# Performance work log

Hardware: AMD Instinct MI355X
Metric: run time of the kernel (lower is better)

The kernel has to match this reference:

```python
import jax, jax.numpy as jnp
import numpy as np

N = 100000
E = 1600000
IN_C = 128
HID = 32
HEADS = 4
NUM_CLASSES = 16
NEG_SLOPE = 0.2


def setup_inputs() -> dict:
    key = jax.random.key(0)
    ks = jax.random.split(key, 10)
    x = jax.random.normal(ks[0], (N, IN_C), dtype=jnp.float32)
    edge_index = jax.random.randint(ks[1], (2, E), 0, N, dtype=jnp.int32)
    s1 = 1.0 / np.sqrt(IN_C)
    s2 = 1.0 / np.sqrt(HID * HEADS)
    W1 = jax.random.normal(ks[2], (IN_C, HEADS * HID), dtype=jnp.float32) * s1
    att_src1 = jax.random.normal(ks[3], (HEADS, HID), dtype=jnp.float32) * s1
    att_dst1 = jax.random.normal(ks[4], (HEADS, HID), dtype=jnp.float32) * s1
    b1 = jnp.zeros((HEADS * HID,), dtype=jnp.float32)
    W2 = jax.random.normal(ks[5], (HEADS * HID, NUM_CLASSES), dtype=jnp.float32) * s2
    att_src2 = jax.random.normal(ks[6], (1, NUM_CLASSES), dtype=jnp.float32) * s2
    att_dst2 = jax.random.normal(ks[7], (1, NUM_CLASSES), dtype=jnp.float32) * s2
    b2 = jnp.zeros((NUM_CLASSES,), dtype=jnp.float32)
    return {"x": x, "edge_index": edge_index,
            "W1": W1, "att_src1": att_src1, "att_dst1": att_dst1, "b1": b1,
            "W2": W2, "att_src2": att_src2, "att_dst2": att_dst2, "b2": b2}


def _gat_conv(x, src, dst, W, att_src, att_dst, b):
    # PyG GATConv: shared linear for src/dst, additive attention, segment softmax over dst.
    n = x.shape[0]
    H, C = att_src.shape
    h = (x @ W).reshape(n, H, C)                       # [N, H, C]
    a_s = jnp.einsum('nhc,hc->nh', h, att_src)          # [N, H]
    a_d = jnp.einsum('nhc,hc->nh', h, att_dst)          # [N, H]
    e = a_s[src] + a_d[dst]                             # [E, H]
    e = jnp.where(e >= 0, e, NEG_SLOPE * e)             # leaky_relu(0.2)
    # numerically stable segment softmax over destination node groups
    e_max = jax.ops.segment_max(e, dst, num_segments=n)
    e_exp = jnp.exp(e - e_max[dst])
    denom = jax.ops.segment_sum(e_exp, dst, num_segments=n)
    alpha = e_exp / denom[dst]                          # [E, H]
    msg = h[src] * alpha[:, :, None]                    # [E, H, C]
    out = jax.ops.segment_sum(msg, dst, num_segments=n) # [N, H, C]
    return out.reshape(n, H * C) + b


def reference(x, edge_index, W1, att_src1, att_dst1, b1, W2, att_src2, att_dst2, b2):
    n = x.shape[0]
    # add_self_loops=True (PyG default), same augmented edge set for both layers
    loop = jnp.arange(n, dtype=edge_index.dtype)
    src = jnp.concatenate([edge_index[0], loop])
    dst = jnp.concatenate([edge_index[1], loop])
    h = _gat_conv(x, src, dst, W1, att_src1, att_dst1, b1)
    h = jax.nn.elu(h)
    out = _gat_conv(h, src, dst, W2, att_src2, att_dst2, b2)
    return out
```

## Files before the change

kernel.cpp:

```cpp
#include <hip/hip_runtime.h>
#include <hip/hip_bf16.h>
#include <math.h>


typedef unsigned short u16;
typedef unsigned int u32;
typedef __attribute__((ext_vector_type(8))) short bf16x8;
typedef __attribute__((ext_vector_type(4))) float f32x4;

__device__ __forceinline__ float eluf(float v) { return v > 0.f ? v : expm1f(v); }
__device__ __forceinline__ u16 f2bf(float f) {
    u32 u = __float_as_uint(f);
    u += 0x7fff + ((u >> 16) & 1);
    return (u16)(u >> 16);
}
__device__ __forceinline__ float bf2f(u16 u) {
    return __uint_as_float(((u32)u) << 16);
}
__device__ __forceinline__ float expleaky(float e) {
    float m = e >= 0.f ? 1.44269504f : 0.28853901f;
    return exp2f(e * m);
}

__global__ __launch_bounds__(256) void ksetup(
    const float* __restrict__ W1, const float* __restrict__ W2,
    const float* __restrict__ ats2, const float* __restrict__ atd2,
    u16* __restrict__ w1fh, u16* __restrict__ w1fl,
    float* __restrict__ u, float* __restrict__ v, u16* __restrict__ w2tb,
    int* __restrict__ deg, int N)
{
    const int b = blockIdx.x, tid = threadIdx.x;
    if (b < 64) {
        int idx = b * 256 + tid;
        int j = idx & 7, l = (idx >> 3) & 63, q = (idx >> 9) & 3, ct = idx >> 11;
        int k = q * 32 + (l >> 4) * 8 + j;
        int n = ct * 16 + (l & 15);
        float w = W1[k * 128 + n];
        u16 hv = f2bf(w);
        w1fh[idx] = hv;
        w1fl[idx] = f2bf(w - bf2f(hv));
    } else if (b == 64) {
        if (tid < 128) {
            float su = 0.f, sv = 0.f;
            #pragma unroll
            for (int j = 0; j < 16; ++j) {
                float w = W2[tid * 16 + j];
                su = fmaf(w, ats2[j], su);
                sv = fmaf(w, atd2[j], sv);
                w2tb[j * 128 + tid] = f2bf(w);
            }
            u[tid] = su; v[tid] = sv;
        }
    } else {
        int z = (b - 65) * 1024 + tid * 4;
        if (z < N) *(int4*)&deg[z] = make_int4(0, 0, 0, 0);
    }
}

#define REPSTRIDE 136
__global__ __launch_bounds__(256) void mega1(
    const float* __restrict__ x, const u16* __restrict__ w1fh,
    const u16* __restrict__ w1fl,
    const float* __restrict__ att_s, const float* __restrict__ att_d,
    u16* __restrict__ h1b, float* __restrict__ as1, float* __restrict__ ad1,
    int N,
    const int* __restrict__ ei, int* __restrict__ deg, int* __restrict__ rank,
    int E, int grid)
{
    __shared__ union {
        struct { u16 lh[8192]; u16 ll[8192]; } w;
        u16 rep[16384];
    } sm;
    const int tid = threadIdx.x;

    for (int e = blockIdx.x * 256 + tid; e < E; e += grid * 256) {
        int dd = ei[E + e];
        rank[e] = atomicAdd(&deg[dd], 1);
    }

    const int wv = tid >> 6, lane = tid & 63;
    const int base = blockIdx.x * 64 + wv * 16;
    const int m = lane & 15, quad = lane >> 4;

    int arow = base + m;
    if (arow >= N) arow = 0;
    const float* xr = &x[(size_t)arow * 128 + quad * 8];
    bf16x8 ah[4], al[4];
    #pragma unroll
    for (int q = 0; q < 4; ++q) {
        float4 f0 = *(const float4*)&xr[q * 32];
        float4 f1 = *(const float4*)&xr[q * 32 + 4];
        float fv[8] = {f0.x, f0.y, f0.z, f0.w, f1.x, f1.y, f1.z, f1.w};
        union { u16 us[8]; bf16x8 v; } hh, lu;
        #pragma unroll
        for (int j = 0; j < 8; ++j) {
            u16 h = f2bf(fv[j]);
            hh.us[j] = h;
            lu.us[j] = f2bf(fv[j] - bf2f(h));
        }
        ah[q] = hh.v; al[q] = lu.v;
    }

    f32x4 accs[8];
    for (int p = 0; p < 2; ++p) {
        __syncthreads();
        #pragma unroll
        for (int i = 0; i < 4; ++i) {
            int fi = (tid + i * 256) * 8;
            *(uint4*)&sm.w.lh[fi] = *(const uint4*)&w1fh[p * 8192 + fi];
            *(uint4*)&sm.w.ll[fi] = *(const uint4*)&w1fl[p * 8192 + fi];
        }
        __syncthreads();
        #pragma unroll
        for (int ctl = 0; ctl < 4; ++ctl) {
            f32x4 acc = {0.f, 0.f, 0.f, 0.f};
            #pragma unroll
            for (int q = 0; q < 4; ++q) {
                const int off = ((ctl * 4 + q) * 64 + lane) * 8;
                bf16x8 bh = *(const bf16x8*)&sm.w.lh[off];
                bf16x8 bl = *(const bf16x8*)&sm.w.ll[off];
                acc = __builtin_amdgcn_mfma_f32_16x16x32_bf16(ah[q], bh, acc, 0, 0, 0);
                acc = __builtin_amdgcn_mfma_f32_16x16x32_bf16(al[q], bh, acc, 0, 0, 0);
                acc = __builtin_amdgcn_mfma_f32_16x16x32_bf16(ah[q], bl, acc, 0, 0, 0);
            }
            accs[p * 4 + ctl] = acc;
        }
    }

    #pragma unroll
    for (int h = 0; h < 4; ++h) {
        const float cs0 = att_s[h * 32 + m];
        const float cs1 = att_s[h * 32 + 16 + m];
        const float cd0 = att_d[h * 32 + m];
        const float cd1 = att_d[h * 32 + 16 + m];
        float sp[4], dp[4];
        #pragma unroll
        for (int r = 0; r < 4; ++r) {
            sp[r] = fmaf(accs[2 * h][r], cs0, accs[2 * h + 1][r] * cs1);
            dp[r] = fmaf(accs[2 * h][r], cd0, accs[2 * h + 1][r] * cd1);
        }
        #pragma unroll
        for (int r = 0; r < 4; ++r) {
            sp[r] += __shfl_xor(sp[r], 1); sp[r] += __shfl_xor(sp[r], 2);
            sp[r] += __shfl_xor(sp[r], 4); sp[r] += __shfl_xor(sp[r], 8);
            dp[r] += __shfl_xor(dp[r], 1); dp[r] += __shfl_xor(dp[r], 2);
            dp[r] += __shfl_xor(dp[r], 4); dp[r] += __shfl_xor(dp[r], 8);
        }
        if (m == 0) {
            #pragma unroll
            for (int r = 0; r < 4; ++r) {
                int rr = base + quad * 4 + r;
                if (rr < N) {
                    as1[rr * 4 + h] = sp[r];
                    ad1[rr * 4 + h] = dp[r];
                }
            }
        }
    }

    __syncthreads();
    u16* rep = sm.rep + wv * (16 * REPSTRIDE);
    #pragma unroll
    for (int ct = 0; ct < 8; ++ct) {
        #pragma unroll
        for (int r = 0; r < 4; ++r)
            rep[(quad * 4 + r) * REPSTRIDE + ct * 16 + m] = f2bf(accs[ct][r]);
    }
    const int rr0 = lane >> 2, cc = lane & 3;
    #pragma unroll
    for (int round = 0; round < 4; ++round) {
        int chunk = cc + 4 * round;
        uint4 vv = *(const uint4*)&rep[rr0 * REPSTRIDE + chunk * 8];
        int grow = base + rr0;
        if (grow < N)
            *(uint4*)&h1b[(size_t)grow * 128 + chunk * 8] = vv;
    }
}

__global__ __launch_bounds__(256) void kscan1(
    const int* __restrict__ deg, int* __restrict__ rowptr,
    int* __restrict__ bsum, int N)
{
    __shared__ int lds[256];
    const int t = threadIdx.x;
    const int base = blockIdx.x * 1024 + t * 4;
    int v[4];
    int s = 0;
    #pragma unroll
    for (int j = 0; j < 4; ++j) {
        v[j] = (base + j < N) ? deg[base + j] : 0;
        s += v[j];
    }
    lds[t] = s;
    __syncthreads();
    for (int off = 1; off < 256; off <<= 1) {
        int y = (t >= off) ? lds[t - off] : 0;
        __syncthreads();
        lds[t] += y;
        __syncthreads();
    }
    int run = lds[t] - s;
    #pragma unroll
    for (int j = 0; j < 4; ++j) {
        if (base + j < N) rowptr[base + j] = run;
        run += v[j];
    }
    if (t == 255) bsum[blockIdx.x] = lds[255];
}

__global__ __launch_bounds__(128) void kscan2(int* __restrict__ bsum, int NB)
{
    __shared__ int lds[128];
    const int t = threadIdx.x;
    int v = (t < NB) ? bsum[t] : 0;
    lds[t] = v;
    __syncthreads();
    for (int off = 1; off < 128; off <<= 1) {
        int y = (t >= off) ? lds[t - off] : 0;
        __syncthreads();
        lds[t] += y;
        __syncthreads();
    }
    if (t < NB) bsum[t] = lds[t] - v;
}

__global__ __launch_bounds__(256) void kscat(
    const int* __restrict__ ei, const int* __restrict__ rowptr,
    const int* __restrict__ bsum, const int* __restrict__ rank,
    int* __restrict__ colidx, int E)
{
    int e = blockIdx.x * 256 + threadIdx.x;
    if (e >= E) return;
    int s = ei[e], d = ei[E + e];
    colidx[rowptr[d] + bsum[d >> 10] + rank[e]] = s;
}

__global__ __launch_bounds__(256) void kg1(
    const int* __restrict__ rowptr, const int* __restrict__ bsum,
    const int* __restrict__ colidx,
    const u16* __restrict__ h1b, const float* __restrict__ as1,
    const float* __restrict__ ad1, const float* __restrict__ b1,
    const float* __restrict__ u, const float* __restrict__ v,
    u16* __restrict__ x2b, float* __restrict__ as2, float* __restrict__ ad2,
    int N, int E)
{
    const int d = blockIdx.x * 4 + (threadIdx.x >> 6);
    if (d >= N) return;
    const int lane = threadIdx.x & 63;
    const int c = lane * 2;
    const int headB = lane >> 4;
    const int headA = lane & 3;
    const int eA = lane >> 2;

    const float adA = ad1[d * 4 + headA];
    const float wself = expleaky(as1[d * 4 + headB] + ad1[d * 4 + headB]);
    u32 hd = *(const u32*)&h1b[(d << 7) + c];
    float accx = wself * bf2f((u16)hd);
    float accy = wself * bf2f((u16)(hd >> 16));
    float den = wself;

    int i0r = rowptr[d] + bsum[d >> 10];
    int i1r = (d + 1 == N) ? E : rowptr[d + 1] + bsum[(d + 1) >> 10];
    const int i0 = __builtin_amdgcn_readfirstlane(i0r);
    const int i1 = __builtin_amdgcn_readfirstlane(i1r);

    for (int i = i0; i < i1; i += 16) {
        const int nb = min(16, i1 - i);
        const int ii = i + eA;
        const int iic = ii < i1 ? ii : i0;
        int sAv = colidx[iic];
        float wA = expleaky(as1[(sAv << 2) + headA] + adA);
        wA = (ii < i1) ? wA : 0.f;
        int e = 0;
        for (; e + 8 <= nb; e += 8) {
            int s0 = colidx[i + e + 0];
            int s1 = colidx[i + e + 1];
            int s2 = colidx[i + e + 2];
            int s3 = colidx[i + e + 3];
            int s4 = colidx[i + e + 4];
            int s5 = colidx[i + e + 5];
            int s6 = colidx[i + e + 6];
            int s7 = colidx[i + e + 7];
            float w0 = __shfl(wA, ((e + 0) << 2) + headB);
            float w1 = __shfl(wA, ((e + 1) << 2) + headB);
            float w2 = __shfl(wA, ((e + 2) << 2) + headB);
            float w3 = __shfl(wA, ((e + 3) << 2) + headB);
            float w4 = __shfl(wA, ((e + 4) << 2) + headB);
            float w5 = __shfl(wA, ((e + 5) << 2) + headB);
            float w6 = __shfl(wA, ((e + 6) << 2) + headB);
            float w7 = __shfl(wA, ((e + 7) << 2) + headB);
            u32 v0 = *(const u32*)&h1b[(s0 << 7) + c];
            u32 v1 = *(const u32*)&h1b[(s1 << 7) + c];
            u32 v2 = *(const u32*)&h1b[(s2 << 7) + c];
            u32 v3 = *(const u32*)&h1b[(s3 << 7) + c];
            u32 v4 = *(const u32*)&h1b[(s4 << 7) + c];
            u32 v5 = *(const u32*)&h1b[(s5 << 7) + c];
            u32 v6 = *(const u32*)&h1b[(s6 << 7) + c];
            u32 v7 = *(const u32*)&h1b[(s7 << 7) + c];
            accx = fmaf(w0, bf2f((u16)v0), accx); accy = fmaf(w0, bf2f((u16)(v0 >> 16)), accy);
            accx = fmaf(w1, bf2f((u16)v1), accx); accy = fmaf(w1, bf2f((u16)(v1 >> 16)), accy);
            accx = fmaf(w2, bf2f((u16)v2), accx); accy = fmaf(w2, bf2f((u16)(v2 >> 16)), accy);
            accx = fmaf(w3, bf2f((u16)v3), accx); accy = fmaf(w3, bf2f((u16)(v3 >> 16)), accy);
            accx = fmaf(w4, bf2f((u16)v4), accx); accy = fmaf(w4, bf2f((u16)(v4 >> 16)), accy);
            accx = fmaf(w5, bf2f((u16)v5), accx); accy = fmaf(w5, bf2f((u16)(v5 >> 16)), accy);
            accx = fmaf(w6, bf2f((u16)v6), accx); accy = fmaf(w6, bf2f((u16)(v6 >> 16)), accy);
            accx = fmaf(w7, bf2f((u16)v7), accx); accy = fmaf(w7, bf2f((u16)(v7 >> 16)), accy);
            den += ((w0 + w1) + (w2 + w3)) + ((w4 + w5) + (w6 + w7));
        }
        for (; e < nb; ++e) {
            int s = colidx[i + e];
            float w = __shfl(wA, (e << 2) + headB);
            u32 hv = *(const u32*)&h1b[(s << 7) + c];
            accx = fmaf(w, bf2f((u16)hv), accx);
            accy = fmaf(w, bf2f((u16)(hv >> 16)), accy);
            den += w;
        }
    }

    const float inv = 1.f / den;
    const float2 bv = *(const float2*)&b1[c];
    const float x2a = eluf(fmaf(accx, inv, bv.x));
    const float x2c = eluf(fmaf(accy, inv, bv.y));

    u32 pk = ((u32)f2bf(x2c) << 16) | (u32)f2bf(x2a);
    *(u32*)&x2b[(d << 7) + c] = pk;

    const float2 uv = *(const float2*)&u[c];
    const float2 vv = *(const float2*)&v[c];
    float sA = fmaf(x2a, uv.x, x2c * uv.y);
    float sB = fmaf(x2a, vv.x, x2c * vv.y);
    #pragma unroll
    for (int m = 1; m < 64; m <<= 1) {
        sA += __shfl_xor(sA, m);
        sB += __shfl_xor(sB, m);
    }
    if (lane == 0) { as2[d] = sA; ad2[d] = sB; }
}

__global__ __launch_bounds__(256) void kh2(
    const u16* __restrict__ x2b, const u16* __restrict__ w2tb,
    u16* __restrict__ h2b, int N)
{
    const int wv = threadIdx.x >> 6, lane = threadIdx.x & 63;
    const int n0 = blockIdx.x * 64 + wv * 16;
    if (n0 >= N) return;
    const int m = lane & 15;
    const int kq = lane >> 4;
    bf16x8 bfr[4];
    #pragma unroll
    for (int q = 0; q < 4; ++q)
        bfr[q] = *(const bf16x8*)&w2tb[m * 128 + q * 32 + kq * 8];

    int ar = n0 + m;
    if (ar >= N) ar = N - 1;
    const u16* arow = &x2b[((size_t)ar << 7) + kq * 8];
    f32x4 acc = {0.f, 0.f, 0.f, 0.f};
    #pragma unroll
    for (int q = 0; q < 4; ++q) {
        bf16x8 af = *(const bf16x8*)&arow[q * 32];
        acc = __builtin_amdgcn_mfma_f32_16x16x32_bf16(af, bfr[q], acc, 0, 0, 0);
    }
    #pragma unroll
    for (int r = 0; r < 4; ++r) {
        int rr = n0 + kq * 4 + r;
        if (rr < N) h2b[((size_t)rr << 4) + m] = f2bf(acc[r]);
    }
}

__global__ __launch_bounds__(256) void kg2(
    const int* __restrict__ rowptr, const int* __restrict__ bsum,
    const int* __restrict__ colidx,
    const u16* __restrict__ h2b, const float* __restrict__ as2,
    const float* __restrict__ ad2, const float* __restrict__ b2,
    float* __restrict__ out, int N, int E)
{
    const int d = blockIdx.x * 4 + (threadIdx.x >> 6);
    if (d >= N) return;
    const int lane = threadIdx.x & 63;
    const int ch = lane & 7, g = lane >> 3;

    const float ad_d = ad2[d];
    float acc0 = 0.f, acc1 = 0.f, den = 0.f;
    int i0r = rowptr[d] + bsum[d >> 10];
    int i1r = (d + 1 == N) ? E : rowptr[d + 1] + bsum[(d + 1) >> 10];
    const int i0 = __builtin_amdgcn_readfirstlane(i0r);
    const int i1 = __builtin_amdgcn_readfirstlane(i1r);

    for (int i = i0; i < i1; i += 64) {
        const int nb = min(64, i1 - i);
        const int idx = i + lane;
        const int idxc = idx < i1 ? idx : i0;
        int sA = colidx[idxc];
        float wA = expleaky(as2[sA] + ad_d);
        wA = (idx < i1) ? wA : 0.f;
        const int kU = (nb + 7) >> 3;
        for (int k = 0; k < kU; ++k) {
            int e = g + 8 * k;
            int ec = e < nb ? e : 0;
            float w = __shfl(wA, ec);
            int s = __shfl(sA, ec);
            if (e >= nb) w = 0.f;
            u32 hv = *(const u32*)&h2b[(s << 4) + ch * 2];
            acc0 = fmaf(w, bf2f((u16)hv), acc0);
            acc1 = fmaf(w, bf2f((u16)(hv >> 16)), acc1);
            den += w;
        }
    }
    acc0 += __shfl_xor(acc0, 8); acc0 += __shfl_xor(acc0, 16); acc0 += __shfl_xor(acc0, 32);
    acc1 += __shfl_xor(acc1, 8); acc1 += __shfl_xor(acc1, 16); acc1 += __shfl_xor(acc1, 32);
    den  += __shfl_xor(den, 8);  den  += __shfl_xor(den, 16);  den  += __shfl_xor(den, 32);

    const float wself = expleaky(as2[d] + ad_d);
    u32 hd = *(const u32*)&h2b[(d << 4) + ch * 2];
    acc0 = fmaf(wself, bf2f((u16)hd), acc0);
    acc1 = fmaf(wself, bf2f((u16)(hd >> 16)), acc1);
    den += wself;
    if (g == 0) {
        float2 ov = {acc0 / den + b2[ch * 2], acc1 / den + b2[ch * 2 + 1]};
        *(float2*)&out[(d << 4) + ch * 2] = ov;
    }
}

extern "C" void kernel_launch(void* const* d_in, const int* in_sizes, int n_in,
                              void* d_out, int out_size, void* d_ws, size_t ws_size,
                              hipStream_t stream) {
    const float* x    = (const float*)d_in[0];
    const int*   ei   = (const int*)d_in[1];
    const float* W1   = (const float*)d_in[2];
    const float* ats1 = (const float*)d_in[3];
    const float* atd1 = (const float*)d_in[4];
    const float* b1   = (const float*)d_in[5];
    const float* W2   = (const float*)d_in[6];
    const float* ats2 = (const float*)d_in[7];
    const float* atd2 = (const float*)d_in[8];
    const float* b2   = (const float*)d_in[9];
    float* out = (float*)d_out;
    const int N = in_sizes[0] / 128;
    const int E = in_sizes[1] / 2;

    u16* h1b   = (u16*)d_ws;
    u16* x2b   = h1b + (size_t)N * 128;
    u16* h2b   = x2b + (size_t)N * 128;
    u16* w2tb  = h2b + (size_t)N * 16;
    u16* w1fh  = w2tb + 2048;
    u16* w1fl  = w1fh + 16384;
    float* as1 = (float*)(w1fl + 16384);
    float* ad1 = as1 + (size_t)N * 4;
    float* as2 = ad1 + (size_t)N * 4;
    float* ad2 = as2 + N;
    float* u   = ad2 + N;
    float* v   = u + 128;
    int* deg    = (int*)(v + 128);
    int* rowptr = deg + ((N + 7) & ~3);
    int* bsum   = rowptr + ((N + 7) & ~3);
    int* colidx = bsum + 128;
    int* rank   = colidx + E;

    const int NB  = (N + 1023) / 1024;
    const int Bh1 = (N + 63) / 64;

    hipLaunchKernelGGL(ksetup, dim3(65 + NB), dim3(256), 0, stream,
                       W1, W2, ats2, atd2, w1fh, w1fl, u, v, w2tb, deg, N);
    hipLaunchKernelGGL(mega1, dim3(Bh1), dim3(256), 0, stream,
                       x, w1fh, w1fl, ats1, atd1, h1b, as1, ad1, N,
                       ei, deg, rank, E, Bh1);
    hipLaunchKernelGGL(kscan1, dim3(NB), dim3(256), 0, stream,
                       deg, rowptr, bsum, N);
    hipLaunchKernelGGL(kscan2, dim3(1), dim3(128), 0, stream, bsum, NB);
    hipLaunchKernelGGL(kscat, dim3((E + 255) / 256), dim3(256), 0, stream,
                       ei, rowptr, bsum, rank, colidx, E);
    hipLaunchKernelGGL(kg1, dim3((N + 3) / 4), dim3(256), 0, stream,
                       rowptr, bsum, colidx, h1b, as1, ad1, b1, u, v,
                       x2b, as2, ad2, N, E);
    hipLaunchKernelGGL(kh2, dim3((N + 63) / 64), dim3(256), 0, stream,
                       x2b, w2tb, h2b, N);
    hipLaunchKernelGGL(kg2, dim3((N + 3) / 4), dim3(256), 0, stream,
                       rowptr, bsum, colidx, h2b, as2, ad2, b2, out, N, E);
}
```

Before: 340.5 us.

## Split per-node degree counters into 16 sub-counters to cut atomic contention

Replaces the single per-destination degree counter with 16 sub-counters per node, chosen by edge block, so atomics on the same node are spread out. The scan kernel now prefix-sums the 16 sub-counters per node in place, and the scatter adds the sub-counter offset when it places each edge. The degree-counting loop is also unrolled four ways so loads and atomics are batched, and the h1b store is remapped so each row's chunks are written contiguously. In exchange the counter array grows 16x, which means more zeroing and scan traffic.

```diff
diff --git a/kernel.cpp b/kernel.cpp
--- a/kernel.cpp
+++ b/kernel.cpp
@@ -27,7 +27,7 @@
     const float* __restrict__ ats2, const float* __restrict__ atd2,
     u16* __restrict__ w1fh, u16* __restrict__ w1fl,
     float* __restrict__ u, float* __restrict__ v, u16* __restrict__ w2tb,
-    int* __restrict__ deg, int N)
+    int* __restrict__ degR, int N)
 {
     const int b = blockIdx.x, tid = threadIdx.x;
     if (b < 64) {
@@ -53,7 +53,7 @@
         }
     } else {
         int z = (b - 65) * 1024 + tid * 4;
-        if (z < N) *(int4*)&deg[z] = make_int4(0, 0, 0, 0);
+        if (z < N * 16) *(int4*)&degR[z] = make_int4(0, 0, 0, 0);
     }
 }
 
@@ -64,7 +64,7 @@
     const float* __restrict__ att_s, const float* __restrict__ att_d,
     u16* __restrict__ h1b, float* __restrict__ as1, float* __restrict__ ad1,
     int N,
-    const int* __restrict__ ei, int* __restrict__ deg, int* __restrict__ rank,
+    const int* __restrict__ ei, int* __restrict__ degR, int* __restrict__ rank,
     int E, int grid)
 {
     __shared__ union {
@@ -73,9 +73,27 @@
     } sm;
     const int tid = threadIdx.x;
 
-    for (int e = blockIdx.x * 256 + tid; e < E; e += grid * 256) {
-        int dd = ei[E + e];
-        rank[e] = atomicAdd(&deg[dd], 1);
+    {
+        const int st = grid * 256;
+        const int e0 = blockIdx.x * 256 + tid;
+        const int ea = e0, eb = e0 + st, ec = e0 + 2 * st, ed = e0 + 3 * st;
+        int da = (ea < E) ? ei[E + ea] : -1;
+        int db = (eb < E) ? ei[E + eb] : -1;
+        int dc = (ec < E) ? ei[E + ec] : -1;
+        int dd = (ed < E) ? ei[E + ed] : -1;
+        int ra = 0, rb = 0, rc = 0, rd = 0;
+        if (da >= 0) ra = atomicAdd(&degR[da * 16 + ((ea >> 8) & 15)], 1);
+        if (db >= 0) rb = atomicAdd(&degR[db * 16 + ((eb >> 8) & 15)], 1);
+        if (dc >= 0) rc = atomicAdd(&degR[dc * 16 + ((ec >> 8) & 15)], 1);
+        if (dd >= 0) rd = atomicAdd(&degR[dd * 16 + ((ed >> 8) & 15)], 1);
+        if (da >= 0) rank[ea] = ra;
+        if (db >= 0) rank[eb] = rb;
+        if (dc >= 0) rank[ec] = rc;
+        if (dd >= 0) rank[ed] = rd;
+        for (int e = e0 + 4 * st; e < E; e += st) {
+            int d2 = ei[E + e];
+            rank[e] = atomicAdd(&degR[d2 * 16 + ((e >> 8) & 15)], 1);
+        }
     }
 
     const int wv = tid >> 6, lane = tid & 63;
@@ -166,30 +184,49 @@
         for (int r = 0; r < 4; ++r)
             rep[(quad * 4 + r) * REPSTRIDE + ct * 16 + m] = f2bf(accs[ct][r]);
     }
-    const int rr0 = lane >> 2, cc = lane & 3;
+    const int chunk = lane & 15;
     #pragma unroll
     for (int round = 0; round < 4; ++round) {
-        int chunk = cc + 4 * round;
-        uint4 vv = *(const uint4*)&rep[rr0 * REPSTRIDE + chunk * 8];
-        int grow = base + rr0;
+        int row = round * 4 + (lane >> 4);
+        uint4 vv = *(const uint4*)&rep[row * REPSTRIDE + chunk * 8];
+        int grow = base + row;
         if (grow < N)
             *(uint4*)&h1b[(size_t)grow * 128 + chunk * 8] = vv;
     }
 }
 
 __global__ __launch_bounds__(256) void kscan1(
-    const int* __restrict__ deg, int* __restrict__ rowptr,
+    int* __restrict__ degR, int* __restrict__ rowptr,
     int* __restrict__ bsum, int N)
 {
     __shared__ int lds[256];
     const int t = threadIdx.x;
     const int base = blockIdx.x * 1024 + t * 4;
-    int v[4];
+    int tot[4];
     int s = 0;
     #pragma unroll
     for (int j = 0; j < 4; ++j) {
-        v[j] = (base + j < N) ? deg[base + j] : 0;
-        s += v[j];
+        int node = base + j;
+        int sum = 0;
+        if (node < N) {
+            int4 c[4];
+            #pragma unroll
+            for (int q = 0; q < 4; ++q) c[q] = *(int4*)&degR[node * 16 + q * 4];
+            int vals[16] = {c[0].x, c[0].y, c[0].z, c[0].w,
+                            c[1].x, c[1].y, c[1].z, c[1].w,
+                            c[2].x, c[2].y, c[2].z, c[2].w,
+                            c[3].x, c[3].y, c[3].z, c[3].w};
+            int run = 0;
+            #pragma unroll
+            for (int q = 0; q < 16; ++q) { int cv = vals[q]; vals[q] = run; run += cv; }
+            sum = run;
+            #pragma unroll
+            for (int q = 0; q < 4; ++q) {
+                int4 pv = {vals[q * 4], vals[q * 4 + 1], vals[q * 4 + 2], vals[q * 4 + 3]};
+                *(int4*)&degR[node * 16 + q * 4] = pv;
+            }
+        }
+        tot[j] = sum; s += sum;
     }
     lds[t] = s;
     __syncthreads();
@@ -203,7 +240,7 @@
     #pragma unroll
     for (int j = 0; j < 4; ++j) {
         if (base + j < N) rowptr[base + j] = run;
-        run += v[j];
+        run += tot[j];
     }
     if (t == 255) bsum[blockIdx.x] = lds[255];
 }
@@ -227,12 +264,13 @@
 __global__ __launch_bounds__(256) void kscat(
     const int* __restrict__ ei, const int* __restrict__ rowptr,
     const int* __restrict__ bsum, const int* __restrict__ rank,
-    int* __restrict__ colidx, int E)
+    const int* __restrict__ degR, int* __restrict__ colidx, int E)
 {
     int e = blockIdx.x * 256 + threadIdx.x;
     if (e >= E) return;
     int s = ei[e], d = ei[E + e];
-    colidx[rowptr[d] + bsum[d >> 10] + rank[e]] = s;
+    int r = (e >> 8) & 15;
+    colidx[rowptr[d] + bsum[d >> 10] + degR[d * 16 + r] + rank[e]] = s;
 }
 
 __global__ __launch_bounds__(256) void kg1(
@@ -450,25 +488,26 @@
     float* ad2 = as2 + N;
     float* u   = ad2 + N;
     float* v   = u + 128;
-    int* deg    = (int*)(v + 128);
-    int* rowptr = deg + ((N + 7) & ~3);
+    int* degR   = (int*)(v + 128);
+    int* rowptr = degR + (size_t)N * 16;
     int* bsum   = rowptr + ((N + 7) & ~3);
     int* colidx = bsum + 128;
     int* rank   = colidx + E;
 
     const int NB  = (N + 1023) / 1024;
+    const int NBZ = (N * 16 + 1023) / 1024;
     const int Bh1 = (N + 63) / 64;
 
-    hipLaunchKernelGGL(ksetup, dim3(65 + NB), dim3(256), 0, stream,
-                       W1, W2, ats2, atd2, w1fh, w1fl, u, v, w2tb, deg, N);
+    hipLaunchKernelGGL(ksetup, dim3(65 + NBZ), dim3(256), 0, stream,
+                       W1, W2, ats2, atd2, w1fh, w1fl, u, v, w2tb, degR, N);
     hipLaunchKernelGGL(mega1, dim3(Bh1), dim3(256), 0, stream,
                        x, w1fh, w1fl, ats1, atd1, h1b, as1, ad1, N,
-                       ei, deg, rank, E, Bh1);
+                       ei, degR, rank, E, Bh1);
     hipLaunchKernelGGL(kscan1, dim3(NB), dim3(256), 0, stream,
-                       deg, rowptr, bsum, N);
+                       degR, rowptr, bsum, N);
     hipLaunchKernelGGL(kscan2, dim3(1), dim3(128), 0, stream, bsum, NB);
     hipLaunchKernelGGL(kscat, dim3((E + 255) / 256), dim3(256), 0, stream,
-                       ei, rowptr, bsum, rank, colidx, E);
+                       ei, rowptr, bsum, rank, degR, colidx, E);
     hipLaunchKernelGGL(kg1, dim3((N + 3) / 4), dim3(256), 0, stream,
                        rowptr, bsum, colidx, h1b, as1, ad1, b1, u, v,
                        x2b, as2, ad2, N, E);
```

Measured after the change: 368.9 us. 1.08x slower.
